# Performance work log

Hardware: AMD Instinct MI355X
Metric: run time of the kernel (lower is better)

Reference implementation:

```python
import jax, jax.numpy as jnp
import numpy as np

BN_EPS = 1e-5
BIND_CHAN = 4  # hparams.MODEL.LEARNABLE_OFFSET.BIND_CHAN


def conv1x1(x, w, b):
    # x: [B,C,H,W], w: [O,C], b: [O]
    return jnp.einsum('bchw,oc->bohw', x, w) + b[None, :, None, None]


def bn_train(x, gamma, beta):
    # training-mode batch norm over (B,H,W) per channel
    mean = jnp.mean(x, axis=(0, 2, 3), keepdims=True)
    var = jnp.var(x, axis=(0, 2, 3), keepdims=True)
    xn = (x - mean) * jax.lax.rsqrt(var + BN_EPS)
    return xn * gamma[None, :, None, None] + beta[None, :, None, None]


def displace_channel(x, offsets):
    # x: [B,C,H,W]; offsets: [C,2] (dy,dx) per channel, continuous.
    # out[b,c,y,x] = bilinear sample of x[b,c] at (y+dy_c, x+dx_c), zeros outside.
    B, C, H, W = x.shape
    dy, dx = offsets[:, 0], offsets[:, 1]
    fy, fx = jnp.floor(dy), jnp.floor(dx)
    wy, wx = dy - fy, dx - fx          # fractional weights, [C]
    iy, ix = fy.astype(jnp.int32), fx.astype(jnp.int32)
    chan = jnp.arange(C)[:, None, None]

    def shifted(oy, ox):
        ys = jnp.arange(H)[None, :] + oy[:, None]   # [C,H]
        xs = jnp.arange(W)[None, :] + ox[:, None]   # [C,W]
        valid = ((ys >= 0) & (ys < H))[:, :, None] & ((xs >= 0) & (xs < W))[:, None, :]
        ysc = jnp.clip(ys, 0, H - 1)
        xsc = jnp.clip(xs, 0, W - 1)
        g = x[:, chan, ysc[:, :, None], xsc[:, None, :]]   # [B,C,H,W]
        return g * valid.astype(x.dtype)[None]

    w00 = ((1 - wy) * (1 - wx))[None, :, None, None]
    w01 = ((1 - wy) * wx)[None, :, None, None]
    w10 = (wy * (1 - wx))[None, :, None, None]
    w11 = (wy * wx)[None, :, None, None]
    return (w00 * shifted(iy, ix) + w01 * shifted(iy, ix + 1)
            + w10 * shifted(iy + 1, ix) + w11 * shifted(iy + 1, ix + 1))


def setup_inputs() -> dict:
    key = jax.random.key(0)
    ks = jax.random.split(key, 12)
    B, Cin, H, W = 16, 64, 128, 128
    Cd, Cout = 128, 64
    n_off = Cd // BIND_CHAN  # 32
    s_in = 1.0 / np.sqrt(Cin)
    s_d = 1.0 / np.sqrt(Cd)
    return {
        'x': jax.random.normal(ks[0], (B, Cin, H, W), jnp.float32),
        'pre_w': jax.random.uniform(ks[1], (Cd, Cin), jnp.float32, -s_in, s_in),
        'pre_b': jax.random.uniform(ks[2], (Cd,), jnp.float32, -s_in, s_in),
        'post_w': jax.random.uniform(ks[3], (Cout, Cd), jnp.float32, -s_d, s_d),
        'post_b': jax.random.uniform(ks[4], (Cout,), jnp.float32, -s_d, s_d),
        'atten_w': jax.random.uniform(ks[5], (Cd, Cin), jnp.float32, -s_in, s_in),
        'atten_b': jax.random.uniform(ks[6], (Cd,), jnp.float32, -s_in, s_in),
        'atten_bn_g': jnp.ones((Cd,), jnp.float32),
        'atten_bn_b': jnp.zeros((Cd,), jnp.float32),
        'offsets': jax.random.normal(ks[7], (n_off, 2), jnp.float32) * 3.0,
        'bn_g': jnp.ones((Cout,), jnp.float32),
        'bn_b': jnp.zeros((Cout,), jnp.float32),
    }


def reference(x, pre_w, pre_b, post_w, post_b, atten_w, atten_b,
              atten_bn_g, atten_bn_b, offsets, bn_g, bn_b):
    # pre_offset conv1x1
    out_pre = conv1x1(x, pre_w, pre_b)                        # [B,Cd,H,W]
    # DisplaceChannel: each offset shared by BIND_CHAN consecutive channels
    off_per_chan = jnp.repeat(offsets, BIND_CHAN, axis=0)     # [Cd,2]
    out_dis = displace_channel(out_pre, off_per_chan)
    # Attention branch: conv1x1 -> BN -> Softplus -> SpaceNormalization
    a = conv1x1(x, atten_w, atten_b)
    a = bn_train(a, atten_bn_g, atten_bn_b)
    a = jax.nn.softplus(a)
    out_atten = a / jnp.sum(a, axis=(2, 3), keepdims=True)    # spatial normalization
    # post_offset conv1x1 on gated displaced features
    out_post = conv1x1(out_atten * out_dis, post_w, post_b)
    # residual (inplanes == outplanes, stride 1 -> no downsample) + BN + ReLU
    out_skip = x + out_post
    return jax.nn.relu(bn_train(out_skip, bn_g, bn_b))
```

## Files before the change

### kernel.cpp

```cpp
#include <hip/hip_runtime.h>

#define HWSZ   16384
#define CIN    64
#define CD     128
#define COUT   64
#define BN_EPS 1e-5f

typedef __attribute__((ext_vector_type(8))) short short8x;
typedef __attribute__((ext_vector_type(4))) float floatx4;

#define WS_WT1   0
#define WS_WTP   16384
#define WS_DISP  24576
#define WS_ASTAT 25344
#define WS_OSTAT 25600
#define WS_SPAT  25728
#define WS_BIG   32768
#define WS_TOTAL_BYTES ((size_t)(32768 + 16777216) * 4)

__device__ __forceinline__ unsigned short f2bf(float f) {
    unsigned int u = __float_as_uint(f);
    u += 0x7fff + ((u >> 16) & 1);
    return (unsigned short)(u >> 16);
}
__device__ __forceinline__ float bf2f(unsigned short s) {
    return __uint_as_float(((unsigned int)s) << 16);
}
__device__ __forceinline__ float softplus_fast(float x) {
    return fmaxf(x, 0.f) + __logf(1.f + __expf(-fabsf(x)));
}
__device__ __forceinline__ float block_reduce(float v, float* sc) {
    #pragma unroll
    for (int off = 32; off >= 1; off >>= 1) v += __shfl_xor(v, off, 64);
    int wv = threadIdx.x >> 6, ln = threadIdx.x & 63;
    if (ln == 0) sc[wv] = v;
    __syncthreads();
    float r = (threadIdx.x < 4) ? sc[threadIdx.x] : 0.f;
    r += __shfl_xor(r, 1, 64);
    r += __shfl_xor(r, 2, 64);
    return r;
}

__global__ __launch_bounds__(256) void prep_kernel(
        const float* __restrict__ pre_w, const float* __restrict__ atten_w,
        const float* __restrict__ post_w, const float* __restrict__ offsets,
        float* __restrict__ ws) {
    int tid = blockIdx.x * 256 + threadIdx.x;
    unsigned short* wAB = (unsigned short*)(ws + WS_WT1);
    unsigned short* wP  = (unsigned short*)(ws + WS_WTP);
    float* disp = ws + WS_DISP;
    if (tid < 16384) {
        int o = tid >> 6, c = tid & 63;
        float v = (o < 128) ? pre_w[o * 64 + c] : atten_w[(o - 128) * 64 + c];
        wAB[tid] = f2bf(v);
    } else if (tid < 24576) {
        int k = tid - 16384;
        int o = k >> 7, c = k & 127;
        wP[k] = f2bf(post_w[o * 128 + c]);
    } else if (tid < 24704) {
        int c = tid - 24576;
        float dy = offsets[(c >> 2) * 2 + 0];
        float dx = offsets[(c >> 2) * 2 + 1];
        float fy = floorf(dy), fx = floorf(dx);
        float wy = dy - fy, wx = dx - fx;
        float* d = disp + c * 6;
        d[0] = fy; d[1] = fx;
        d[2] = (1.f - wy) * (1.f - wx);
        d[3] = (1.f - wy) * wx;
        d[4] = wy * (1.f - wx);
        d[5] = wy * wx;
    }
}

__global__ __launch_bounds__(256) void conv_pre_mfma(
        const float* __restrict__ x, const unsigned short* __restrict__ wAB,
        const float* __restrict__ pre_b, const float* __restrict__ atten_b,
        unsigned short* __restrict__ out_pre, unsigned short* __restrict__ a_out) {
    __shared__ unsigned short xT[64 * 72];
    int t = threadIdx.x;
    int wv = t >> 6, ln = t & 63;
    int P0 = blockIdx.x * 64;
    int b = P0 >> 14, poff = P0 & 16383;
    const float* xg = x + (size_t)b * CIN * HWSZ + poff;
    int c = ln;
    #pragma unroll
    for (int k = 0; k < 4; ++k) {
        int px = wv * 16 + k * 4;
        float4 v = *(const float4*)(xg + (size_t)c * HWSZ + px);
        xT[(px + 0) * 72 + c] = f2bf(v.x);
        xT[(px + 1) * 72 + c] = f2bf(v.y);
        xT[(px + 2) * 72 + c] = f2bf(v.z);
        xT[(px + 3) * 72 + c] = f2bf(v.w);
    }
    __syncthreads();
    int o0 = wv * 64;
    short8x afrag[4][2];
    #pragma unroll
    for (int oi = 0; oi < 4; ++oi)
        #pragma unroll
        for (int kk = 0; kk < 2; ++kk) {
            int row = o0 + oi * 16 + (ln & 15);
            int kcol = kk * 32 + (ln >> 4) * 8;
            afrag[oi][kk] = *(const short8x*)(wAB + row * 64 + kcol);
        }
    floatx4 acc[4][4];
    #pragma unroll
    for (int oi = 0; oi < 4; ++oi) {
        int og = o0 + oi * 16;
        const float* bias = (og < 128) ? (pre_b + og) : (atten_b + og - 128);
        float4 b4 = *(const float4*)(bias + (ln >> 4) * 4);
        #pragma unroll
        for (int pi = 0; pi < 4; ++pi)
            acc[oi][pi] = floatx4{b4.x, b4.y, b4.z, b4.w};
    }
    #pragma unroll
    for (int kk = 0; kk < 2; ++kk)
        #pragma unroll
        for (int pi = 0; pi < 4; ++pi) {
            short8x bfrag = *(const short8x*)((const char*)xT +
                    (pi * 16 + (ln & 15)) * 144 + (kk * 32 + (ln >> 4) * 8) * 2);
            #pragma unroll
            for (int oi = 0; oi < 4; ++oi)
                acc[oi][pi] = __builtin_amdgcn_mfma_f32_16x16x32_bf16(
                        afrag[oi][kk], bfrag, acc[oi][pi], 0, 0, 0);
        }
    #pragma unroll
    for (int oi = 0; oi < 4; ++oi) {
        int og = o0 + oi * 16;
        unsigned short* dst = (og < 128) ? out_pre : a_out;
        int ob = (og < 128) ? og : og - 128;
        #pragma unroll
        for (int pi = 0; pi < 4; ++pi) {
            int px = poff + pi * 16 + (ln & 15);
            #pragma unroll
            for (int r = 0; r < 4; ++r) {
                int o = ob + (ln >> 4) * 4 + r;
                dst[((size_t)b * CD + o) * HWSZ + px] = f2bf(acc[oi][pi][r]);
            }
        }
    }
}

__global__ __launch_bounds__(256) void chan_stats_bf16(
        const unsigned short* __restrict__ src, float* __restrict__ stats) {
    __shared__ float sc1[8], sc2[8];
    int c = blockIdx.x, b = blockIdx.y;
    const unsigned short* base = src + ((size_t)b * CD + c) * HWSZ;
    int t = threadIdx.x;
    float sum = 0.f, sq = 0.f;
    #pragma unroll
    for (int i = 0; i < 8; ++i) {
        uint4 v = *(const uint4*)(base + i * 2048 + t * 8);
        unsigned int u[4] = {v.x, v.y, v.z, v.w};
        #pragma unroll
        for (int k = 0; k < 4; ++k) {
            float lo = bf2f((unsigned short)(u[k] & 0xffff));
            float hi = bf2f((unsigned short)(u[k] >> 16));
            sum += lo + hi;
            sq  += lo * lo + hi * hi;
        }
    }
    sum = block_reduce(sum, sc1);
    __syncthreads();
    sq = block_reduce(sq, sc2);
    if (t == 0) {
        atomicAdd(&stats[c * 2 + 0], sum);
        atomicAdd(&stats[c * 2 + 1], sq);
    }
}

__global__ __launch_bounds__(256) void bn_softplus(
        unsigned int* __restrict__ a, const float* __restrict__ stats,
        const float* __restrict__ g, const float* __restrict__ bb,
        float* __restrict__ spat) {
    __shared__ float sc[8];
    int bc = blockIdx.x;
    int c = bc & 127;
    const float N = 262144.f;
    float mean = stats[c * 2] / N;
    float var  = stats[c * 2 + 1] / N - mean * mean;
    float rstd = rsqrtf(var + BN_EPS);
    float scl = rstd * g[c];
    float shf = bb[c] - mean * scl;
    unsigned int* base = a + (size_t)bc * (HWSZ / 2);
    int t = threadIdx.x;
    float lsum = 0.f;
    #pragma unroll 2
    for (int i = 0; i < 8; ++i) {
        uint4 v = *(uint4*)(base + i * 1024 + t * 4);
        unsigned int* u = (unsigned int*)&v;
        #pragma unroll
        for (int k = 0; k < 4; ++k) {
            float lo = bf2f((unsigned short)(u[k] & 0xffff));
            float hi = bf2f((unsigned short)(u[k] >> 16));
            lo = softplus_fast(lo * scl + shf);
            hi = softplus_fast(hi * scl + shf);
            lsum += lo + hi;
            u[k] = (unsigned int)f2bf(lo) | ((unsigned int)f2bf(hi) << 16);
        }
        *(uint4*)(base + i * 1024 + t * 4) = v;
    }
    lsum = block_reduce(lsum, sc);
    if (t == 0) spat[bc] = lsum;
}

struct Win9 { float v0,v1,v2,v3,v4,v5,v6,v7,v8; };
__device__ __forceinline__ Win9 extract9(uint4 qa, uint4 qb, bool s4, int sh) {
    unsigned long long A0 = ((unsigned long long)qa.y << 32) | qa.x;
    unsigned long long A1 = ((unsigned long long)qa.w << 32) | qa.z;
    unsigned long long A2 = ((unsigned long long)qb.y << 32) | qb.x;
    unsigned long long A3 = ((unsigned long long)qb.w << 32) | qb.z;
    unsigned long long B0 = s4 ? A1 : A0;
    unsigned long long B1 = s4 ? A2 : A1;
    unsigned long long B2 = s4 ? A3 : A2;
    unsigned long long r0 = sh ? ((B0 >> sh) | (B1 << (64 - sh))) : B0;
    unsigned long long r1 = sh ? ((B1 >> sh) | (B2 << (64 - sh))) : B1;
    unsigned int v8w = (unsigned int)(sh ? (B2 >> sh) : B2);
    Win9 w;
    w.v0 = bf2f((unsigned short)(r0 >>  0)); w.v1 = bf2f((unsigned short)(r0 >> 16));
    w.v2 = bf2f((unsigned short)(r0 >> 32)); w.v3 = bf2f((unsigned short)(r0 >> 48));
    w.v4 = bf2f((unsigned short)(r1 >>  0)); w.v5 = bf2f((unsigned short)(r1 >> 16));
    w.v6 = bf2f((unsigned short)(r1 >> 32)); w.v7 = bf2f((unsigned short)(r1 >> 48));
    w.v8 = bf2f((unsigned short)(v8w & 0xffff));
    return w;
}

__global__ __launch_bounds__(256) void displace_mul(
        unsigned short* __restrict__ pre, const unsigned short* __restrict__ a_sp,
        const float* __restrict__ spat, const float* __restrict__ disp) {
    __shared__ unsigned short img[128 * 136];
    int bc = blockIdx.x;
    int cc = bc & 127;
    const float* d = disp + cc * 6;
    int iy = (int)d[0], ix = (int)d[1];
    float w00 = d[2], w01 = d[3], w10 = d[4], w11 = d[5];
    float inv = 1.f / spat[bc];
    unsigned short* pb = pre + (size_t)bc * HWSZ;
    const unsigned short* ab = a_sp + (size_t)bc * HWSZ;
    int t = threadIdx.x;
    #pragma unroll
    for (int i = 0; i < 8; ++i) {
        int px = i * 2048 + t * 8;
        uint4 v = *(const uint4*)(pb + px);
        int y = px >> 7, xx = px & 127;
        *(uint4*)&img[y * 136 + xx] = v;
    }
    __syncthreads();
    int s = ix & 7;
    int ix8 = ix - s;
    int sh = (s & 3) * 16;
    bool s4 = s >= 4;
    for (int i = 0; i < 8; ++i) {
        int px = i * 2048 + t * 8;
        int y = px >> 7, x0 = px & 127;
        int yy0 = y + iy, yy1 = yy0 + 1;
        float wA0 = (yy0 >= 0 && yy0 < 128) ? w00 : 0.f;
        float wA1 = (yy0 >= 0 && yy0 < 128) ? w01 : 0.f;
        float wB0 = (yy1 >= 0 && yy1 < 128) ? w10 : 0.f;
        float wB1 = (yy1 >= 0 && yy1 < 128) ? w11 : 0.f;
        int yc0 = min(max(yy0, 0), 127), yc1 = min(max(yy1, 0), 127);
        int w0 = x0 + ix8;
        uint4 z = {0u, 0u, 0u, 0u};
        uint4 qa0 = (w0 >= 0 && w0 <= 120)         ? *(const uint4*)&img[yc0 * 136 + w0]     : z;
        uint4 qa1 = (w0 + 8 >= 0 && w0 + 8 <= 120) ? *(const uint4*)&img[yc0 * 136 + w0 + 8] : z;
        uint4 qb0 = (w0 >= 0 && w0 <= 120)         ? *(const uint4*)&img[yc1 * 136 + w0]     : z;
        uint4 qb1 = (w0 + 8 >= 0 && w0 + 8 <= 120) ? *(const uint4*)&img[yc1 * 136 + w0 + 8] : z;
        Win9 va = extract9(qa0, qa1, s4, sh);
        Win9 vb = extract9(qb0, qb1, s4, sh);
        float dv0 = wA0*va.v0 + wA1*va.v1 + wB0*vb.v0 + wB1*vb.v1;
        float dv1 = wA0*va.v1 + wA1*va.v2 + wB0*vb.v1 + wB1*vb.v2;
        float dv2 = wA0*va.v2 + wA1*va.v3 + wB0*vb.v2 + wB1*vb.v3;
        float dv3 = wA0*va.v3 + wA1*va.v4 + wB0*vb.v3 + wB1*vb.v4;
        float dv4 = wA0*va.v4 + wA1*va.v5 + wB0*vb.v4 + wB1*vb.v5;
        float dv5 = wA0*va.v5 + wA1*va.v6 + wB0*vb.v5 + wB1*vb.v6;
        float dv6 = wA0*va.v6 + wA1*va.v7 + wB0*vb.v6 + wB1*vb.v7;
        float dv7 = wA0*va.v7 + wA1*va.v8 + wB0*vb.v7 + wB1*vb.v8;
        uint4 av = *(const uint4*)(ab + px);
        unsigned int au[4] = {av.x, av.y, av.z, av.w};
        float a0 = bf2f((unsigned short)(au[0] & 0xffff)) * inv;
        float a1 = bf2f((unsigned short)(au[0] >> 16)) * inv;
        float a2 = bf2f((unsigned short)(au[1] & 0xffff)) * inv;
        float a3 = bf2f((unsigned short)(au[1] >> 16)) * inv;
        float a4 = bf2f((unsigned short)(au[2] & 0xffff)) * inv;
        float a5 = bf2f((unsigned short)(au[2] >> 16)) * inv;
        float a6 = bf2f((unsigned short)(au[3] & 0xffff)) * inv;
        float a7 = bf2f((unsigned short)(au[3] >> 16)) * inv;
        uint4 o;
        o.x = (unsigned int)f2bf(dv0 * a0) | ((unsigned int)f2bf(dv1 * a1) << 16);
        o.y = (unsigned int)f2bf(dv2 * a2) | ((unsigned int)f2bf(dv3 * a3) << 16);
        o.z = (unsigned int)f2bf(dv4 * a4) | ((unsigned int)f2bf(dv5 * a5) << 16);
        o.w = (unsigned int)f2bf(dv6 * a6) | ((unsigned int)f2bf(dv7 * a7) << 16);
        *(uint4*)(pb + px) = o;
    }
}

__global__ __launch_bounds__(256) void conv_post_mfma(
        const unsigned short* __restrict__ m, const unsigned short* __restrict__ wP,
        const float* __restrict__ post_b, const float* __restrict__ x,
        unsigned short* __restrict__ skipS) {
    __shared__ unsigned short mT[128 * 128];
    int t = threadIdx.x;
    int P0 = blockIdx.x * 128;
    int b = P0 >> 14, poff = P0 & 16383;
    int cl = t & 31, q = t >> 5;
    #pragma unroll
    for (int pass = 0; pass < 4; ++pass) {
        int c = cl + pass * 32;
        const unsigned short* mrow = m + ((size_t)b * CD + c) * HWSZ + poff;
        #pragma unroll
        for (int h = 0; h < 2; ++h) {
            int px0 = h * 64 + q * 8;
            uint4 v = *(const uint4*)(mrow + px0);
            unsigned int u[4] = {v.x, v.y, v.z, v.w};
            #pragma unroll
            for (int j = 0; j < 8; ++j) {
                unsigned short val = (unsigned short)((u[j >> 1] >> ((j & 1) * 16)) & 0xffff);
                int byteoff = (px0 + j) * 256 + ((c * 2) ^ (j << 4));
                *(unsigned short*)((char*)mT + byteoff) = val;
            }
        }
    }
    __syncthreads();
    int ln = t & 63, wv = t >> 6;
    int o0 = (wv >> 1) * 32;
    int ph = (wv & 1) * 64;
    short8x aw[2][4];
    #pragma unroll
    for (int oi = 0; oi < 2; ++oi)
        #pragma unroll
        for (int kk = 0; kk < 4; ++kk)
            aw[oi][kk] = *(const short8x*)(wP + (o0 + oi * 16 + (ln & 15)) * 128 + kk * 32 + (ln >> 4) * 8);
    floatx4 acc[2][4];
    #pragma unroll
    for (int oi = 0; oi < 2; ++oi)
        #pragma unroll
        for (int pi = 0; pi < 4; ++pi) acc[oi][pi] = floatx4{0.f, 0.f, 0.f, 0.f};
    #pragma unroll
    for (int kk = 0; kk < 4; ++kk)
        #pragma unroll
        for (int pi = 0; pi < 4; ++pi) {
            int px = ph + pi * 16 + (ln & 15);
            int cb = kk * 64 + (ln >> 4) * 16;
            short8x bf = *(const short8x*)((const char*)mT + px * 256 + (cb ^ ((px & 7) << 4)));
            #pragma unroll
            for (int oi = 0; oi < 2; ++oi)
                acc[oi][pi] = __builtin_amdgcn_mfma_f32_16x16x32_bf16(aw[oi][kk], bf, acc[oi][pi], 0, 0, 0);
        }
    #pragma unroll
    for (int oi = 0; oi < 2; ++oi) {
        float4 b4 = *(const float4*)(post_b + o0 + oi * 16 + (ln >> 4) * 4);
        float bb[4] = {b4.x, b4.y, b4.z, b4.w};
        #pragma unroll
        for (int pi = 0; pi < 4; ++pi) {
            int pxg = poff + ph + pi * 16 + (ln & 15);
            #pragma unroll
            for (int r = 0; r < 4; ++r) {
                int o = o0 + oi * 16 + (ln >> 4) * 4 + r;
                float val = acc[oi][pi][r] + bb[r] + x[((size_t)b * COUT + o) * HWSZ + pxg];
                skipS[((size_t)b * CD + o) * HWSZ + pxg] = f2bf(val);
            }
        }
    }
}

__global__ __launch_bounds__(256) void bn_relu_out(
        const unsigned short* __restrict__ skipS, float* __restrict__ out,
        const float* __restrict__ stats, const float* __restrict__ g,
        const float* __restrict__ bb) {
    const float N = 262144.f;
    int t = threadIdx.x;
    #pragma unroll
    for (int k = 0; k < 4; ++k) {
        size_t gidx = (size_t)blockIdx.x * 1024 + k * 256 + t;
        size_t e = gidx * 8;
        int b = (int)(e >> 20);
        int c = (int)(e >> 14) & 63;
        int px = (int)(e & 16383);
        float mean = stats[c * 2] / N;
        float rstd = rsqrtf(stats[c * 2 + 1] / N - mean * mean + BN_EPS);
        float gc = g[c], bbc = bb[c];
        uint4 v = *(const uint4*)(skipS + ((size_t)b * CD + c) * HWSZ + px);
        unsigned int u[4] = {v.x, v.y, v.z, v.w};
        float4 o0, o1;
        float* op[8] = {&o0.x, &o0.y, &o0.z, &o0.w, &o1.x, &o1.y, &o1.z, &o1.w};
        #pragma unroll
        for (int j = 0; j < 8; ++j) {
            float val = bf2f((unsigned short)((u[j >> 1] >> ((j & 1) * 16)) & 0xffff));
            *op[j] = fmaxf((val - mean) * rstd * gc + bbc, 0.f);
        }
        *(float4*)(out + e) = o0;
        *(float4*)(out + e + 4) = o1;
    }
}

extern "C" void kernel_launch(void* const* d_in, const int* in_sizes, int n_in,
                              void* d_out, int out_size, void* d_ws, size_t ws_size,
                              hipStream_t stream) {
    const float* x          = (const float*)d_in[0];
    const float* pre_w      = (const float*)d_in[1];
    const float* pre_b      = (const float*)d_in[2];
    const float* post_w     = (const float*)d_in[3];
    const float* post_b     = (const float*)d_in[4];
    const float* atten_w    = (const float*)d_in[5];
    const float* atten_b    = (const float*)d_in[6];
    const float* atten_bn_g = (const float*)d_in[7];
    const float* atten_bn_b = (const float*)d_in[8];
    const float* offsets    = (const float*)d_in[9];
    const float* bn_g       = (const float*)d_in[10];
    const float* bn_b       = (const float*)d_in[11];
    float* out = (float*)d_out;
    float* ws  = (float*)d_ws;

    if (ws_size < WS_TOTAL_BYTES) return;

    unsigned short* wAB = (unsigned short*)(ws + WS_WT1);
    unsigned short* wP  = (unsigned short*)(ws + WS_WTP);
    float* disp    = ws + WS_DISP;
    float* a_stats = ws + WS_ASTAT;
    float* o_stats = ws + WS_OSTAT;
    float* spat    = ws + WS_SPAT;
    unsigned short* big   = (unsigned short*)(ws + WS_BIG);
    unsigned short* a_buf = (unsigned short*)d_out;

    hipMemsetAsync((void*)a_stats, 0, 384 * sizeof(float), stream);

    prep_kernel<<<97, 256, 0, stream>>>(pre_w, atten_w, post_w, offsets, ws);
    conv_pre_mfma<<<4096, 256, 0, stream>>>(x, wAB, pre_b, atten_b, big, a_buf);
    chan_stats_bf16<<<dim3(128, 16), 256, 0, stream>>>(a_buf, a_stats);
    bn_softplus<<<2048, 256, 0, stream>>>((unsigned int*)a_buf, a_stats, atten_bn_g, atten_bn_b, spat);
    displace_mul<<<2048, 256, 0, stream>>>(big, a_buf, spat, disp);
    conv_post_mfma<<<2048, 256, 0, stream>>>(big, wP, post_b, x, big);
    chan_stats_bf16<<<dim3(64, 16), 256, 0, stream>>>(big, o_stats);
    bn_relu_out<<<2048, 256, 0, stream>>>(big, out, o_stats, bn_g, bn_b);
}
```

Baseline: 186.7 us.

## Process four pixel tiles per block in conv_pre with double-buffered LDS prefetch

Each block of the first 1x1 conv now handles 256 pixels as four 64-pixel tiles instead of one, with the grid reduced from 4096 to 1024 blocks. Weight fragments and biases are loaded once per block and reused across the four tiles. The next tile's x values are loaded into registers while the current tile's MFMAs and stores run, then written to a second LDS buffer. This trades fewer, longer blocks and more register pressure for less redundant weight loading and some overlap of global loads with compute.

```diff
diff --git a/kernel.cpp b/kernel.cpp
--- a/kernel.cpp
+++ b/kernel.cpp
@@ -76,68 +76,99 @@
         const float* __restrict__ x, const unsigned short* __restrict__ wAB,
         const float* __restrict__ pre_b, const float* __restrict__ atten_b,
         unsigned short* __restrict__ out_pre, unsigned short* __restrict__ a_out) {
-    __shared__ unsigned short xT[64 * 72];
+    __shared__ unsigned short xT[2][64 * 72];
     int t = threadIdx.x;
     int wv = t >> 6, ln = t & 63;
-    int P0 = blockIdx.x * 64;
-    int b = P0 >> 14, poff = P0 & 16383;
+    int b = blockIdx.x >> 6;
+    int poff = (blockIdx.x & 63) << 8;
     const float* xg = x + (size_t)b * CIN * HWSZ + poff;
     int c = ln;
-    #pragma unroll
-    for (int k = 0; k < 4; ++k) {
-        int px = wv * 16 + k * 4;
-        float4 v = *(const float4*)(xg + (size_t)c * HWSZ + px);
-        xT[(px + 0) * 72 + c] = f2bf(v.x);
-        xT[(px + 1) * 72 + c] = f2bf(v.y);
-        xT[(px + 2) * 72 + c] = f2bf(v.z);
-        xT[(px + 3) * 72 + c] = f2bf(v.w);
-    }
-    __syncthreads();
+
     int o0 = wv * 64;
-    short8x afrag[4][2];
+    short8x wfrag[4][2];
     #pragma unroll
     for (int oi = 0; oi < 4; ++oi)
         #pragma unroll
         for (int kk = 0; kk < 2; ++kk) {
             int row = o0 + oi * 16 + (ln & 15);
             int kcol = kk * 32 + (ln >> 4) * 8;
-            afrag[oi][kk] = *(const short8x*)(wAB + row * 64 + kcol);
-        }
-    floatx4 acc[4][4];
+            wfrag[oi][kk] = *(const short8x*)(wAB + row * 64 + kcol);
+        }
+    float4 biasv[4];
     #pragma unroll
     for (int oi = 0; oi < 4; ++oi) {
         int og = o0 + oi * 16;
         const float* bias = (og < 128) ? (pre_b + og) : (atten_b + og - 128);
-        float4 b4 = *(const float4*)(bias + (ln >> 4) * 4);
-        #pragma unroll
-        for (int pi = 0; pi < 4; ++pi)
-            acc[oi][pi] = floatx4{b4.x, b4.y, b4.z, b4.w};
-    }
-    #pragma unroll
-    for (int kk = 0; kk < 2; ++kk)
-        #pragma unroll
-        for (int pi = 0; pi < 4; ++pi) {
-            short8x bfrag = *(const short8x*)((const char*)xT +
-                    (pi * 16 + (ln & 15)) * 144 + (kk * 32 + (ln >> 4) * 8) * 2);
-            #pragma unroll
-            for (int oi = 0; oi < 4; ++oi)
-                acc[oi][pi] = __builtin_amdgcn_mfma_f32_16x16x32_bf16(
-                        afrag[oi][kk], bfrag, acc[oi][pi], 0, 0, 0);
-        }
-    #pragma unroll
-    for (int oi = 0; oi < 4; ++oi) {
-        int og = o0 + oi * 16;
-        unsigned short* dst = (og < 128) ? out_pre : a_out;
-        int ob = (og < 128) ? og : og - 128;
-        #pragma unroll
-        for (int pi = 0; pi < 4; ++pi) {
-            int px = poff + pi * 16 + (ln & 15);
-            #pragma unroll
-            for (int r = 0; r < 4; ++r) {
-                int o = ob + (ln >> 4) * 4 + r;
-                dst[((size_t)b * CD + o) * HWSZ + px] = f2bf(acc[oi][pi][r]);
+        biasv[oi] = *(const float4*)(bias + (ln >> 4) * 4);
+    }
+
+    float4 ld[4];
+    #pragma unroll
+    for (int k = 0; k < 4; ++k)
+        ld[k] = *(const float4*)(xg + (size_t)c * HWSZ + 0 * 64 + wv * 16 + k * 4);
+    #pragma unroll
+    for (int k = 0; k < 4; ++k) {
+        int px = wv * 16 + k * 4;
+        xT[0][(px + 0) * 72 + c] = f2bf(ld[k].x);
+        xT[0][(px + 1) * 72 + c] = f2bf(ld[k].y);
+        xT[0][(px + 2) * 72 + c] = f2bf(ld[k].z);
+        xT[0][(px + 3) * 72 + c] = f2bf(ld[k].w);
+    }
+    __syncthreads();
+
+    #pragma unroll
+    for (int tt = 0; tt < 4; ++tt) {
+        if (tt < 3) {
+            #pragma unroll
+            for (int k = 0; k < 4; ++k)
+                ld[k] = *(const float4*)(xg + (size_t)c * HWSZ + (tt + 1) * 64 + wv * 16 + k * 4);
+        }
+        const unsigned short* buf = xT[tt & 1];
+        floatx4 acc[4][4];
+        #pragma unroll
+        for (int oi = 0; oi < 4; ++oi)
+            #pragma unroll
+            for (int pi = 0; pi < 4; ++pi)
+                acc[oi][pi] = floatx4{biasv[oi].x, biasv[oi].y, biasv[oi].z, biasv[oi].w};
+        #pragma unroll
+        for (int kk = 0; kk < 2; ++kk)
+            #pragma unroll
+            for (int pi = 0; pi < 4; ++pi) {
+                short8x xfrag = *(const short8x*)((const char*)buf +
+                        (pi * 16 + (ln & 15)) * 144 + (kk * 32 + (ln >> 4) * 8) * 2);
+                #pragma unroll
+                for (int oi = 0; oi < 4; ++oi)
+                    acc[oi][pi] = __builtin_amdgcn_mfma_f32_16x16x32_bf16(
+                            wfrag[oi][kk], xfrag, acc[oi][pi], 0, 0, 0);
             }
-        }
+        int ptile = poff + tt * 64;
+        #pragma unroll
+        for (int oi = 0; oi < 4; ++oi) {
+            int og = o0 + oi * 16;
+            unsigned short* dst = (og < 128) ? out_pre : a_out;
+            int ob = (og < 128) ? og : og - 128;
+            #pragma unroll
+            for (int pi = 0; pi < 4; ++pi) {
+                int px = ptile + pi * 16 + (ln & 15);
+                #pragma unroll
+                for (int r = 0; r < 4; ++r) {
+                    int o = ob + (ln >> 4) * 4 + r;
+                    dst[((size_t)b * CD + o) * HWSZ + px] = f2bf(acc[oi][pi][r]);
+                }
+            }
+        }
+        if (tt < 3) {
+            unsigned short* wbuf = xT[(tt + 1) & 1];
+            #pragma unroll
+            for (int k = 0; k < 4; ++k) {
+                int px = wv * 16 + k * 4;
+                wbuf[(px + 0) * 72 + c] = f2bf(ld[k].x);
+                wbuf[(px + 1) * 72 + c] = f2bf(ld[k].y);
+                wbuf[(px + 2) * 72 + c] = f2bf(ld[k].z);
+                wbuf[(px + 3) * 72 + c] = f2bf(ld[k].w);
+            }
+        }
+        __syncthreads();
     }
 }
 
@@ -425,7 +456,7 @@
     hipMemsetAsync((void*)a_stats, 0, 384 * sizeof(float), stream);
 
     prep_kernel<<<97, 256, 0, stream>>>(pre_w, atten_w, post_w, offsets, ws);
-    conv_pre_mfma<<<4096, 256, 0, stream>>>(x, wAB, pre_b, atten_b, big, a_buf);
+    conv_pre_mfma<<<1024, 256, 0, stream>>>(x, wAB, pre_b, atten_b, big, a_buf);
     chan_stats_bf16<<<dim3(128, 16), 256, 0, stream>>>(a_buf, a_stats);
     bn_softplus<<<2048, 256, 0, stream>>>((unsigned int*)a_buf, a_stats, atten_bn_g, atten_bn_b, spat);
     displace_mul<<<2048, 256, 0, stream>>>(big, a_buf, spat, disp);
```

Measured after the change: 180.1 us. 3.5% less time.
